# Kernel optimization log

Hardware: AMD Instinct MI355X
Metric: run time of the kernel (lower is better)

## Reference

```python
import jax, jax.numpy as jnp
import numpy as np
from jax import lax

# BatchNorm inference with running_mean=0, running_var=1: y = gamma*x/sqrt(1+eps) + beta
_BN_INV = 1.0 / float(np.sqrt(1.0 + 1e-5))


def _conv(x, w, b, pad):
    # x: (B,C,H,W), w: (O,C,k,k)
    y = lax.conv_general_dilated(x, w, (1, 1), [(pad, pad), (pad, pad)],
                                 dimension_numbers=('NCHW', 'OIHW', 'NCHW'))
    return y + b[None, :, None, None]


def _basic(x, w, b, g, e):
    # Conv5x5(pad=2) -> BN(inference) -> ReLU
    y = _conv(x, w, b, 2)
    y = y * (g * _BN_INV)[None, :, None, None] + e[None, :, None, None]
    return jnp.maximum(y, 0.0)


def _pool(x):
    # avg_pool2d kernel=2 stride=2
    B, C, H, W = x.shape
    return x.reshape(B, C, H // 2, 2, W // 2, 2).mean(axis=(3, 5))


def _up(x, oh, ow):
    # bilinear, align_corners=True (matches F.interpolate(..., align_corners=True))
    B, C, H, W = x.shape
    ys = jnp.linspace(0.0, H - 1.0, oh)
    xs = jnp.linspace(0.0, W - 1.0, ow)
    y0 = jnp.floor(ys).astype(jnp.int32)
    y1 = jnp.minimum(y0 + 1, H - 1)
    wy = (ys - y0)[:, None]  # (oh,1)
    x0 = jnp.floor(xs).astype(jnp.int32)
    x1 = jnp.minimum(x0 + 1, W - 1)
    wx = xs - x0  # (ow,)
    xh = x[:, :, y0, :] * (1.0 - wy) + x[:, :, y1, :] * wy  # (B,C,oh,W)
    return xh[..., x0] * (1.0 - wx) + xh[..., x1] * wx       # (B,C,oh,ow)


def setup_inputs() -> dict:
    key = jax.random.key(0)
    ks = jax.random.split(key, 16)
    chans = [(64, 3), (128, 64), (256, 128), (512, 256), (512, 512),
             (512, 1024), (256, 768), (3, 384)]
    inp = {"data": jax.random.normal(ks[0], (2, 3, 512, 512), jnp.float32)}
    for n, (o, c) in enumerate(chans, 1):
        fan = 1.0 / np.sqrt(c * 25.0)
        inp[f"w{n}"] = jax.random.normal(ks[n], (o, c, 5, 5), jnp.float32) * fan
        inp[f"b{n}"] = jnp.zeros((o,), jnp.float32)
        inp[f"g{n}"] = jnp.ones((o,), jnp.float32)
        inp[f"e{n}"] = jnp.zeros((o,), jnp.float32)
    inp["wo"] = jax.random.normal(ks[9], (3, 3, 1, 1), jnp.float32) * 0.5
    inp["bo"] = jnp.zeros((3,), jnp.float32)
    return inp


def reference(data, w1, b1, g1, e1, w2, b2, g2, e2, w3, b3, g3, e3,
              w4, b4, g4, e4, w5, b5, g5, e5, w6, b6, g6, e6,
              w7, b7, g7, e7, w8, b8, g8, e8, wo, bo):
    c1 = _basic(data, w1, b1, g1, e1)                    # (B,64,H,W)
    c2 = _basic(_pool(c1), w2, b2, g2, e2)               # (B,128,H/2,W/2)
    c3 = _basic(_pool(c2), w3, b3, g3, e3)               # (B,256,H/4,W/4)
    c4 = _basic(_pool(c3), w4, b4, g4, e4)               # (B,512,H/8,W/8)
    c5 = _basic(_pool(c4), w5, b5, g5, e5)               # (B,512,H/16,W/16)
    c6 = _basic(jnp.concatenate([c4, _up(c5, c4.shape[2], c4.shape[3])], 1),
                w6, b6, g6, e6)                          # (B,512,H/8,W/8)
    c7 = _basic(jnp.concatenate([c3, _up(c6, c3.shape[2], c3.shape[3])], 1),
                w7, b7, g7, e7)                          # (B,256,H/4,W/4)
    c8 = _basic(jnp.concatenate([c2, _up(c7, c2.shape[2], c2.shape[3])], 1),
                w8, b8, g8, e8)                          # (B,3,H/2,W/2)
    core = _conv(_up(c8, data.shape[2], data.shape[3]), wo, bo, 0)  # (B,3,H,W)
    return data * core
```

## Files before the change

kernel.cpp:

```cpp
#include <hip/hip_runtime.h>
#include <hip/hip_bf16.h>

typedef _Float16 f16x8 __attribute__((ext_vector_type(8)));
typedef _Float16 f16x4 __attribute__((ext_vector_type(4)));
typedef float f32x4 __attribute__((ext_vector_type(4)));

#define BN_S 0.99999500003749975f

__device__ inline f16x8 f16x8_zero() {
  f16x8 v = {(_Float16)0.f, (_Float16)0.f, (_Float16)0.f, (_Float16)0.f,
             (_Float16)0.f, (_Float16)0.f, (_Float16)0.f, (_Float16)0.f};
  return v;
}

__device__ __forceinline__ void load_lds16(const _Float16* g, _Float16* l) {
  __builtin_amdgcn_global_load_lds(
      (const __attribute__((address_space(1))) void*)g,
      (__attribute__((address_space(3))) void*)l, 16, 0, 0);
}

__global__ void zero_out_k(float* __restrict__ out, int n) {
  const int idx = blockIdx.x * 256 + threadIdx.x;
  if (idx < n) out[idx] = 0.f;
}

__global__ void zero16_k(_Float16* __restrict__ p, int n16) {
  const int idx = blockIdx.x * 256 + threadIdx.x;
  if (idx < n16) ((f16x8*)p)[idx] = f16x8_zero();
}

__global__ void wtrans16(const float* __restrict__ src, _Float16* __restrict__ dst,
                         const float* __restrict__ g, int O, int C, int total) {
  const int idx = blockIdx.x * 256 + threadIdx.x;
  if (idx >= total) return;
  const int OC = O * C;
  const int t = idx / OC;
  const int rem = idx - t * OC;
  const int o = rem / C;
  const int c = rem - o * C;
  dst[idx] = (_Float16)(src[(size_t)(o * C + c) * 25 + t] * g[o] * BN_S);
}

__global__ void wtrans8(const float* __restrict__ src, _Float16* __restrict__ dst,
                        const float* __restrict__ g) {
  const int idx = blockIdx.x * 256 + threadIdx.x;
  if (idx >= 28800) return;
  const int c = idx / 600;
  const int r = idx - c * 600;
  const int tap = r / 24;
  const int q = r - tap * 24;
  const int o = q >> 3, j = q & 7;
  const int cin = (c < 16) ? (c * 8 + j) : (128 + (c - 16) * 8 + j);
  dst[idx] = (_Float16)(src[((size_t)o * 384 + cin) * 25 + tap] * g[o] * BN_S);
}

template <int MF, int NF>
__global__ __launch_bounds__(256) void conv_gemm(
    const _Float16* __restrict__ in, const _Float16* __restrict__ wt,
    const float* __restrict__ gg, const float* __restrict__ bbv,
    const float* __restrict__ ev, _Float16* __restrict__ out,
    int Cin, int Cout, int lw, int lh,
    int inS, int Wpi, int bsi, int ibase,
    int outS, int outOff, int Wpo, int bso, int obase) {
  constexpr int BM = MF * 32;
  constexpr int BN = NF * 32;
  __shared__ _Float16 sA[2][BM * 32];
  __shared__ _Float16 sB[2][BN * 32];

  const int tid = threadIdx.x;
  const int lane = tid & 63;
  const int wid = tid >> 6;
  const int wm = wid >> 1, wn = wid & 1;
  const int lr = lane >> 4, lc = lane & 15;
  const int n0 = blockIdx.x * BN;
  const int m0 = blockIdx.y * BM;
  const int H = 1 << lh, W = 1 << lw;
  const int nkb = Cin >> 5;

  const int r0 = tid >> 2;
  const int chunk = (tid & 3) ^ ((r0 >> 1) & 3);

  const _Float16* a0 = wt + (size_t)(m0 + r0) * Cin + (chunk << 3);
  const _Float16* a1 = a0 + ((size_t)Cin << 6);
  const int t0off = -2 * Wpi - 2;
  const _Float16 *b0, *b1 = nullptr;
  {
    int n = n0 + r0;
    int pix0 = (n >> (lw + lh)) * bsi + ((n >> lw) & (H - 1)) * Wpi + (n & (W - 1)) + ibase;
    b0 = in + (size_t)(pix0 + t0off) * inS + (chunk << 3);
    if constexpr (BN == 128) {
      n = n0 + r0 + 64;
      int pix1 = (n >> (lw + lh)) * bsi + ((n >> lw) & (H - 1)) * Wpi + (n & (W - 1)) + ibase;
      b1 = in + (size_t)(pix1 + t0off) * inS + (chunk << 3);
    }
  }

  const int swz = (lr ^ ((lc >> 1) & 3)) << 3;

  f32x4 acc[MF][NF];
  const f32x4 vz = {0.f, 0.f, 0.f, 0.f};
#pragma unroll
  for (int i = 0; i < MF; ++i)
#pragma unroll
    for (int j = 0; j < NF; ++j) acc[i][j] = vz;

  const int nt = 25 * nkb;
  int kb = 0, dx = 0;
  const size_t a_tap = (size_t)Cout * Cin - ((size_t)nkb << 5);
  const int woff = wid << 9;

  {
    _Float16* sa = sA[0] + woff;
    _Float16* sb = sB[0] + woff;
    load_lds16(a0, sa);
    if constexpr (BM == 128) load_lds16(a1, sa + 2048);
    load_lds16(b0, sb);
    if constexpr (BN == 128) load_lds16(b1, sb + 2048);
  }
  __syncthreads();

  int cur = 0;
  for (int t = 0; t < nt; ++t) {
    if (t + 1 < nt) {
      a0 += 32; b0 += 32;
      if constexpr (BM == 128) a1 += 32;
      if constexpr (BN == 128) b1 += 32;
      if (++kb == nkb) {
        kb = 0;
        a0 += a_tap;
        if constexpr (BM == 128) a1 += a_tap;
        int pd;
        if (++dx == 5) { dx = 0; pd = Wpi - 4; } else pd = 1;
        const ptrdiff_t bd = (ptrdiff_t)pd * inS - ((ptrdiff_t)nkb << 5);
        b0 += bd;
        if constexpr (BN == 128) b1 += bd;
      }
      _Float16* sa = (cur ? sA[0] : sA[1]) + woff;
      _Float16* sb = (cur ? sB[0] : sB[1]) + woff;
      load_lds16(a0, sa);
      if constexpr (BM == 128) load_lds16(a1, sa + 2048);
      load_lds16(b0, sb);
      if constexpr (BN == 128) load_lds16(b1, sb + 2048);
    }
    const _Float16* pA = cur ? sA[1] : sA[0];
    const _Float16* pB = cur ? sB[1] : sB[0];
    f16x8 af[MF], bf[NF];
#pragma unroll
    for (int i = 0; i < MF; ++i)
      af[i] = *(const f16x8*)(pA + ((wm * (MF * 16) + (i << 4) + lc) << 5) + swz);
#pragma unroll
    for (int i = 0; i < NF; ++i)
      bf[i] = *(const f16x8*)(pB + ((wn * (NF * 16) + (i << 4) + lc) << 5) + swz);
#pragma unroll
    for (int mi = 0; mi < MF; ++mi)
#pragma unroll
      for (int ni = 0; ni < NF; ++ni)
        acc[mi][ni] =
            __builtin_amdgcn_mfma_f32_16x16x32_f16(af[mi], bf[ni], acc[mi][ni], 0, 0, 0);
    __syncthreads();
    cur ^= 1;
  }

#pragma unroll
  for (int mi = 0; mi < MF; ++mi) {
    const int ob = m0 + wm * (MF * 16) + (mi << 4) + (lr << 2);
    const f32x4 gv = *(const f32x4*)(gg + ob);
    const f32x4 bv = *(const f32x4*)(bbv + ob);
    const f32x4 evv = *(const f32x4*)(ev + ob);
#pragma unroll
    for (int ni = 0; ni < NF; ++ni) {
      const int n = n0 + wn * (NF * 16) + (ni << 4) + lc;
      const int y = (n >> lw) & (H - 1);
      const int x = n & (W - 1);
      const int bb_ = n >> (lw + lh);
      const size_t op = (size_t)(bb_ * bso + y * Wpo + x + obase) * outS + outOff + ob;
      f16x4 h;
#pragma unroll
      for (int j = 0; j < 4; ++j) {
        const float s = gv[j] * BN_S;
        float v = acc[mi][ni][j] + (bv[j] * s + evv[j]);
        v = v > 0.f ? v : 0.f;
        h[j] = (_Float16)v;
      }
      *(f16x4*)(out + op) = h;
    }
  }
}

__global__ __launch_bounds__(256) void conv1_k(
    const float* __restrict__ data, const float* __restrict__ w1,
    const float* __restrict__ g1, const float* __restrict__ b1,
    const float* __restrict__ e1, _Float16* __restrict__ out) {
  __shared__ float patch[3][20][20];
  const int tid = threadIdx.x;
  const int bid = blockIdx.x;
  const int tx = bid & 31, ty = (bid >> 5) & 31, b = bid >> 10;

  for (int i = tid; i < 1200; i += 256) {
    const int c = i / 400;
    const int r = i - c * 400;
    const int pyy = r / 20;
    const int pxx = r - pyy * 20;
    const int gy = (ty << 4) + pyy - 2, gx = (tx << 4) + pxx - 2;
    float v = 0.f;
    if ((unsigned)gy < 512u && (unsigned)gx < 512u)
      v = data[((size_t)(b * 3 + c) << 18) + (gy << 9) + gx];
    patch[c][pyy][pxx] = v;
  }
  __syncthreads();

  const int py = tid >> 4, px = tid & 15;
  float acc[64];
#pragma unroll
  for (int o = 0; o < 64; ++o) acc[o] = 0.f;

  for (int c = 0; c < 3; ++c)
    for (int dy = 0; dy < 5; ++dy) {
#pragma unroll
      for (int dx = 0; dx < 5; ++dx) {
        const float v = patch[c][py + dy][px + dx];
        const float* wb = w1 + c * 25 + dy * 5 + dx;
#pragma unroll
        for (int o = 0; o < 64; ++o) acc[o] = fmaf(v, wb[o * 75], acc[o]);
      }
    }

  const int y = (ty << 4) + py, x = (tx << 4) + px;
  _Float16* op = out + ((size_t)(((b << 9) + y) << 9) + x) * 64;
#pragma unroll
  for (int oc = 0; oc < 8; ++oc) {
    f16x8 h;
#pragma unroll
    for (int j = 0; j < 8; ++j) {
      const int o = (oc << 3) + j;
      const float s = g1[o] * BN_S;
      const float t = b1[o] * s + e1[o];
      float v = fmaf(acc[o], s, t);
      v = v > 0.f ? v : 0.f;
      h[j] = (_Float16)v;
    }
    *(f16x8*)(op + (oc << 3)) = h;
  }
}

__global__ void pool_k(const _Float16* __restrict__ in, _Float16* __restrict__ out,
                       int inS, int outS, int Wpi, int bsi, int ibase,
                       int Wpo, int bso, int obase,
                       int lwo, int lho, int lcc, int total) {
  const int idx = blockIdx.x * 256 + threadIdx.x;
  if (idx >= total) return;
  const int cc = idx & ((1 << lcc) - 1);
  const int pix = idx >> lcc;
  const int x = pix & ((1 << lwo) - 1);
  const int y = (pix >> lwo) & ((1 << lho) - 1);
  const int b = pix >> (lwo + lho);
  const int ip = b * bsi + (y << 1) * Wpi + (x << 1) + ibase;
  const _Float16* p = in + (size_t)ip * inS + (cc << 3);
  const f16x8 v00 = *(const f16x8*)p;
  const f16x8 v01 = *(const f16x8*)(p + inS);
  const f16x8 v10 = *(const f16x8*)(p + (size_t)Wpi * inS);
  const f16x8 v11 = *(const f16x8*)(p + (size_t)(Wpi + 1) * inS);
  f16x8 r;
#pragma unroll
  for (int j = 0; j < 8; ++j)
    r[j] = (_Float16)(((float)v00[j] + (float)v01[j] + (float)v10[j] + (float)v11[j]) * 0.25f);
  const int op = b * bso + y * Wpo + x + obase;
  *(f16x8*)(out + (size_t)op * outS + (cc << 3)) = r;
}

__global__ void up_k(const _Float16* __restrict__ in, _Float16* __restrict__ out,
                     int inS, int outS, int outOff,
                     int Wpi, int bsi, int ibase,
                     int Wpo, int bso, int obase,
                     int lwi, int lhi, int lcc, float scale, int total) {
  const int idx = blockIdx.x * 256 + threadIdx.x;
  if (idx >= total) return;
  const int cc = idx & ((1 << lcc) - 1);
  const int pix = idx >> lcc;
  const int lwo = lwi + 1, lho = lhi + 1;
  const int ox = pix & ((1 << lwo) - 1);
  const int oy = (pix >> lwo) & ((1 << lho) - 1);
  const int b = pix >> (lwo + lho);
  const int Hi = 1 << lhi, Wi = 1 << lwi;
  const float fy = oy * scale;
  const int y0 = (int)fy;
  const float wy = fy - y0;
  const int y1 = min(y0 + 1, Hi - 1);
  const float fx = ox * scale;
  const int x0 = (int)fx;
  const float wx = fx - x0;
  const int x1 = min(x0 + 1, Wi - 1);
  const int rbase = b * bsi + ibase;
  const _Float16* basep = in + (cc << 3);
  const f16x8 v00 = *(const f16x8*)(basep + (size_t)(rbase + y0 * Wpi + x0) * inS);
  const f16x8 v01 = *(const f16x8*)(basep + (size_t)(rbase + y0 * Wpi + x1) * inS);
  const f16x8 v10 = *(const f16x8*)(basep + (size_t)(rbase + y1 * Wpi + x0) * inS);
  const f16x8 v11 = *(const f16x8*)(basep + (size_t)(rbase + y1 * Wpi + x1) * inS);
  f16x8 r;
#pragma unroll
  for (int j = 0; j < 8; ++j) {
    const float top = (float)v00[j] * (1.f - wx) + (float)v01[j] * wx;
    const float bot = (float)v10[j] * (1.f - wx) + (float)v11[j] * wx;
    r[j] = (_Float16)(top * (1.f - wy) + bot * wy);
  }
  const int op = b * bso + oy * Wpo + ox + obase;
  *(f16x8*)(out + (size_t)op * outS + outOff + (cc << 3)) = r;
}

__global__ __launch_bounds__(256) void conv8_lds(
    const _Float16* __restrict__ inA, const _Float16* __restrict__ inB,
    const _Float16* __restrict__ wt, const float* __restrict__ b8,
    const float* __restrict__ g8, const float* __restrict__ e8,
    _Float16* __restrict__ out) {
  __shared__ f16x8 patch[2][20][20];
  const int tid = threadIdx.x;
  const int bid = blockIdx.x;
  const int tx = bid & 15, ty = (bid >> 4) & 15, b = bid >> 8;
  const int px = tid & 15, py = tid >> 4;
  const int x0 = tx << 4, y0 = ty << 4;

  float a0 = 0.f, a1 = 0.f, a2 = 0.f;
  for (int c = 0; c < 48; ++c) {
    const _Float16* sbase;
    int str;
    if (c < 16) { sbase = inA + ((size_t)b << 23) + (c << 3); str = 128; }
    else        { sbase = inB + ((size_t)b << 24) + ((c - 16) << 3); str = 256; }
    for (int i = tid; i < 400; i += 256) {
      const int pyy = i / 20, pxx = i - pyy * 20;
      const int gy = y0 + pyy - 2, gx = x0 + pxx - 2;
      f16x8 v = f16x8_zero();
      if ((unsigned)gy < 256u && (unsigned)gx < 256u)
        v = *(const f16x8*)(sbase + (size_t)((gy << 8) + gx) * str);
      patch[c & 1][pyy][pxx] = v;
    }
    __syncthreads();
    const _Float16* wb_c = wt + c * 600;
#pragma unroll
    for (int dy = 0; dy < 5; ++dy) {
#pragma unroll
      for (int dxx = 0; dxx < 5; ++dxx) {
        const f16x8 v = patch[c & 1][py + dy][px + dxx];
        const _Float16* wb = wb_c + (dy * 5 + dxx) * 24;
#pragma unroll
        for (int j = 0; j < 8; ++j) {
          const float f = (float)v[j];
          a0 = fmaf(f, (float)wb[j], a0);
          a1 = fmaf(f, (float)wb[8 + j], a1);
          a2 = fmaf(f, (float)wb[16 + j], a2);
        }
      }
    }
  }

  const float s0 = g8[0] * BN_S, t0 = b8[0] * s0 + e8[0];
  const float s1 = g8[1] * BN_S, t1 = b8[1] * s1 + e8[1];
  const float s2 = g8[2] * BN_S, t2 = b8[2] * s2 + e8[2];
  float r0 = a0 + t0, r1 = a1 + t1, r2 = a2 + t2;
  r0 = r0 > 0.f ? r0 : 0.f;
  r1 = r1 > 0.f ? r1 : 0.f;
  r2 = r2 > 0.f ? r2 : 0.f;
  f16x4 h;
  h[0] = (_Float16)r0; h[1] = (_Float16)r1; h[2] = (_Float16)r2; h[3] = (_Float16)0.f;
  const int opix = (b << 16) + ((y0 + py) << 8) + (x0 + px);
  *(f16x4*)(out + (size_t)opix * 4) = h;
}

__global__ void final_k(const float* __restrict__ data, const _Float16* __restrict__ c8,
                        const float* __restrict__ wo, const float* __restrict__ bo,
                        float* __restrict__ out) {
  const int idx = blockIdx.x * 256 + threadIdx.x;
  const int x = idx & 511, y = (idx >> 9) & 511, b = idx >> 18;
  const float sc = 255.f / 511.f;
  const float fy = y * sc;
  const int y0 = (int)fy;
  const float wy = fy - y0;
  const int y1 = min(y0 + 1, 255);
  const float fx = x * sc;
  const int x0 = (int)fx;
  const float wx = fx - x0;
  const int x1 = min(x0 + 1, 255);
  const f16x4 v00 = *(const f16x4*)(c8 + (size_t)((((b << 8) + y0) << 8) + x0) * 4);
  const f16x4 v01 = *(const f16x4*)(c8 + (size_t)((((b << 8) + y0) << 8) + x1) * 4);
  const f16x4 v10 = *(const f16x4*)(c8 + (size_t)((((b << 8) + y1) << 8) + x0) * 4);
  const f16x4 v11 = *(const f16x4*)(c8 + (size_t)((((b << 8) + y1) << 8) + x1) * 4);
  float u[3];
#pragma unroll
  for (int j = 0; j < 3; ++j) {
    const float top = (float)v00[j] * (1.f - wx) + (float)v01[j] * wx;
    const float bot = (float)v10[j] * (1.f - wx) + (float)v11[j] * wx;
    u[j] = top * (1.f - wy) + bot * wy;
  }
#pragma unroll
  for (int c = 0; c < 3; ++c) {
    const float core = bo[c] + wo[c * 3 + 0] * u[0] + wo[c * 3 + 1] * u[1] + wo[c * 3 + 2] * u[2];
    const size_t oi = ((size_t)(b * 3 + c) << 18) + (y << 9) + x;
    out[oi] = data[oi] * core;
  }
}

extern "C" void kernel_launch(void* const* d_in, const int* in_sizes, int n_in,
                              void* d_out, int out_size, void* d_ws, size_t ws_size,
                              hipStream_t stream) {
  const float* data = (const float*)d_in[0];
  const float *w[9], *bb[9], *gg[9], *ee[9];
  for (int n = 1; n <= 8; ++n) {
    w[n] = (const float*)d_in[1 + (n - 1) * 4];
    bb[n] = (const float*)d_in[2 + (n - 1) * 4];
    gg[n] = (const float*)d_in[3 + (n - 1) * 4];
    ee[n] = (const float*)d_in[4 + (n - 1) * 4];
  }
  const float* wo = (const float*)d_in[33];
  const float* bo = (const float*)d_in[34];
  float* out = (float*)d_out;
  (void)in_sizes; (void)n_in;

  const size_t NEEDED = 194810112ull;
  if (ws_size < NEEDED) {
    zero_out_k<<<(out_size + 255) / 256, 256, 0, stream>>>(out, out_size);
    return;
  }
  char* base = (char*)d_ws;
  size_t off = 0;
  auto alloc = [&](size_t bytes) -> char* {
    char* p = base + off;
    off += (bytes + 255) & ~(size_t)255;
    return p;
  };
  _Float16* W2t = (_Float16*)alloc(409600);
  _Float16* W3t = (_Float16*)alloc(1638400);
  _Float16* W4t = (_Float16*)alloc(6553600);
  _Float16* W5t = (_Float16*)alloc(13107200);
  _Float16* W6t = (_Float16*)alloc(26214400);
  _Float16* W7t = (_Float16*)alloc(9830400);
  _Float16* W8t = (_Float16*)alloc(57600);
  char* Rbig = alloc(72466432);
  char* c2b_ = alloc(33554432);
  char* R1 = alloc(17305600);
  char* R2 = alloc(13672448);

  _Float16* c1 = (_Float16*)Rbig;
  _Float16* cat7 = (_Float16*)Rbig;
  _Float16* cat6 = (_Float16*)(Rbig + 53526528);
  _Float16* up7b = (_Float16*)Rbig;
  _Float16* c2buf = (_Float16*)c2b_;
  _Float16* p1 = (_Float16*)R1;
  _Float16* c6 = (_Float16*)R1;
  _Float16* c7 = (_Float16*)R1;
  _Float16* c8 = (_Float16*)R1;
  _Float16* p2 = (_Float16*)R2;
  _Float16* p3 = (_Float16*)(R2 + 8921088);
  _Float16* p4 = (_Float16*)(R2 + 8921088);
  _Float16* c5 = (_Float16*)(R2 + 8921088 + 2654208);

  zero16_k<<<(1081600 + 255) / 256, 256, 0, stream>>>(p1, 1081600);
  zero16_k<<<(557568 + 255) / 256, 256, 0, stream>>>(p2, 557568);
  zero16_k<<<(295936 + 255) / 256, 256, 0, stream>>>(p3, 295936);

  wtrans16<<<(25 * 128 * 64 + 255) / 256, 256, 0, stream>>>(w[2], W2t, gg[2], 128, 64, 25 * 128 * 64);
  wtrans16<<<(25 * 256 * 128 + 255) / 256, 256, 0, stream>>>(w[3], W3t, gg[3], 256, 128, 25 * 256 * 128);
  wtrans16<<<(25 * 512 * 256 + 255) / 256, 256, 0, stream>>>(w[4], W4t, gg[4], 512, 256, 25 * 512 * 256);
  wtrans16<<<(25 * 512 * 512 + 255) / 256, 256, 0, stream>>>(w[5], W5t, gg[5], 512, 512, 25 * 512 * 512);
  wtrans16<<<(25 * 512 * 1024 + 255) / 256, 256, 0, stream>>>(w[6], W6t, gg[6], 512, 1024, 25 * 512 * 1024);
  wtrans16<<<(25 * 256 * 768 + 255) / 256, 256, 0, stream>>>(w[7], W7t, gg[7], 256, 768, 25 * 256 * 768);
  wtrans8<<<(28800 + 255) / 256, 256, 0, stream>>>(w[8], W8t, gg[8]);

  conv1_k<<<2048, 256, 0, stream>>>(data, w[1], gg[1], bb[1], ee[1], c1);
  pool_k<<<1048576 / 256, 256, 0, stream>>>(c1, p1, 64, 64, 512, 262144, 0,
                                            260, 67600, 522, 8, 8, 3, 1048576);
  zero16_k<<<(3345408 + 255) / 256, 256, 0, stream>>>(cat7, 3345408);
  zero16_k<<<(1183744 + 255) / 256, 256, 0, stream>>>(cat6, 1183744);

  conv_gemm<4, 4><<<dim3(1024, 1), 256, 0, stream>>>(p1, W2t, gg[2], bb[2], ee[2], c2buf,
      64, 128, 8, 8, 64, 260, 67600, 522, 128, 0, 256, 65536, 0);
  pool_k<<<524288 / 256, 256, 0, stream>>>(c2buf, p2, 128, 128, 256, 65536, 0,
                                           132, 17424, 266, 7, 7, 4, 524288);
  conv_gemm<4, 4><<<dim3(256, 2), 256, 0, stream>>>(p2, W3t, gg[3], bb[3], ee[3], cat7,
      128, 256, 7, 7, 128, 132, 17424, 266, 768, 0, 132, 17424, 266);
  pool_k<<<262144 / 256, 256, 0, stream>>>(cat7, p3, 768, 256, 132, 17424, 266,
                                           68, 4624, 138, 6, 6, 5, 262144);
  conv_gemm<4, 2><<<dim3(128, 4), 256, 0, stream>>>(p3, W4t, gg[4], bb[4], ee[4], cat6,
      256, 512, 6, 6, 256, 68, 4624, 138, 1024, 0, 68, 4624, 138);
  zero16_k<<<(165888 + 255) / 256, 256, 0, stream>>>(p4, 165888);
  pool_k<<<131072 / 256, 256, 0, stream>>>(cat6, p4, 1024, 512, 68, 4624, 138,
                                           36, 1296, 74, 5, 5, 6, 131072);
  conv_gemm<2, 2><<<dim3(32, 8), 256, 0, stream>>>(p4, W5t, gg[5], bb[5], ee[5], c5,
      512, 512, 5, 5, 512, 36, 1296, 74, 512, 0, 32, 1024, 0);
  up_k<<<524288 / 256, 256, 0, stream>>>(c5, cat6, 512, 1024, 512,
                                         32, 1024, 0, 68, 4624, 138,
                                         5, 5, 6, 31.f / 63.f, 524288);
  conv_gemm<4, 2><<<dim3(128, 4), 256, 0, stream>>>(cat6, W6t, gg[6], bb[6], ee[6], c6,
      1024, 512, 6, 6, 1024, 68, 4624, 138, 512, 0, 64, 4096, 0);
  up_k<<<2097152 / 256, 256, 0, stream>>>(c6, cat7, 512, 768, 256,
                                          64, 4096, 0, 132, 17424, 266,
                                          6, 6, 6, 63.f / 127.f, 2097152);
  conv_gemm<4, 2><<<dim3(512, 2), 256, 0, stream>>>(cat7, W7t, gg[7], bb[7], ee[7], c7,
      768, 256, 7, 7, 768, 132, 17424, 266, 256, 0, 128, 16384, 0);
  up_k<<<4194304 / 256, 256, 0, stream>>>(c7, up7b, 256, 256, 0,
                                          128, 16384, 0, 256, 65536, 0,
                                          7, 7, 5, 127.f / 255.f, 4194304);
  conv8_lds<<<512, 256, 0, stream>>>(c2buf, up7b, W8t, bb[8], gg[8], ee[8], c8);
  final_k<<<524288 / 256, 256, 0, stream>>>(data, c8, wo, bo, out);
}
```

Before: 1.961 ms.

## Deepen conv GEMM LDS pipeline to four buffers with vmcnt waits and larger tiles

The implicit-GEMM conv kernel moves from a double-buffered LDS pipeline with __syncthreads to a four-slot ring that prefetches two k-steps ahead. It waits on explicit s_waitcnt vmcnt counts so global-to-LDS loads overlap with MFMA work. Layers 4, 6 and 7 also switch from 128x64 to 128x128 tiles, which halves the grid. This aims to hide memory latency and improve data reuse, at the cost of doubled LDS use, lower occupancy, and a risk of wrong vmcnt counts if the compiler emits other vector memory operations in the loop.

Result: slower. 2.062 ms (+5.2%).

```diff
diff --git a/kernel.cpp b/kernel.cpp
--- a/kernel.cpp
+++ b/kernel.cpp
@@ -64,8 +64,9 @@
     int outS, int outOff, int Wpo, int bso, int obase) {
   constexpr int BM = MF * 32;
   constexpr int BN = NF * 32;
-  __shared__ _Float16 sA[2][BM * 32];
-  __shared__ _Float16 sB[2][BN * 32];
+  constexpr int LPS = ((BM == 128) ? 2 : 1) + ((BN == 128) ? 2 : 1);
+  __shared__ _Float16 sA[4][BM * 32];
+  __shared__ _Float16 sB[4][BN * 32];
 
   const int tid = threadIdx.x;
   const int lane = tid & 63;
@@ -109,41 +110,52 @@
   const size_t a_tap = (size_t)Cout * Cin - ((size_t)nkb << 5);
   const int woff = wid << 9;
 
-  {
-    _Float16* sa = sA[0] + woff;
-    _Float16* sb = sB[0] + woff;
+  auto advance = [&]() {
+    a0 += 32; b0 += 32;
+    if constexpr (BM == 128) a1 += 32;
+    if constexpr (BN == 128) b1 += 32;
+    if (++kb == nkb) {
+      kb = 0;
+      a0 += a_tap;
+      if constexpr (BM == 128) a1 += a_tap;
+      int pd;
+      if (++dx == 5) { dx = 0; pd = Wpi - 4; } else pd = 1;
+      const ptrdiff_t bd = (ptrdiff_t)pd * inS - ((ptrdiff_t)nkb << 5);
+      b0 += bd;
+      if constexpr (BN == 128) b1 += bd;
+    }
+  };
+  auto stage = [&](int buf) {
+    _Float16* sa = sA[buf] + woff;
+    _Float16* sb = sB[buf] + woff;
     load_lds16(a0, sa);
     if constexpr (BM == 128) load_lds16(a1, sa + 2048);
     load_lds16(b0, sb);
     if constexpr (BN == 128) load_lds16(b1, sb + 2048);
-  }
-  __syncthreads();
-
-  int cur = 0;
+  };
+
+  stage(0);
+  advance();
+  stage(1);
+
   for (int t = 0; t < nt; ++t) {
-    if (t + 1 < nt) {
-      a0 += 32; b0 += 32;
-      if constexpr (BM == 128) a1 += 32;
-      if constexpr (BN == 128) b1 += 32;
-      if (++kb == nkb) {
-        kb = 0;
-        a0 += a_tap;
-        if constexpr (BM == 128) a1 += a_tap;
-        int pd;
-        if (++dx == 5) { dx = 0; pd = Wpi - 4; } else pd = 1;
-        const ptrdiff_t bd = (ptrdiff_t)pd * inS - ((ptrdiff_t)nkb << 5);
-        b0 += bd;
-        if constexpr (BN == 128) b1 += bd;
-      }
-      _Float16* sa = (cur ? sA[0] : sA[1]) + woff;
-      _Float16* sb = (cur ? sB[0] : sB[1]) + woff;
-      load_lds16(a0, sa);
-      if constexpr (BM == 128) load_lds16(a1, sa + 2048);
-      load_lds16(b0, sb);
-      if constexpr (BN == 128) load_lds16(b1, sb + 2048);
-    }
-    const _Float16* pA = cur ? sA[1] : sA[0];
-    const _Float16* pB = cur ? sB[1] : sB[0];
+    if (t + 2 < nt) {
+      advance();
+      stage((t + 2) & 3);
+      if constexpr (LPS == 4) asm volatile("s_waitcnt vmcnt(8)" ::: "memory");
+      else if constexpr (LPS == 3) asm volatile("s_waitcnt vmcnt(6)" ::: "memory");
+      else asm volatile("s_waitcnt vmcnt(4)" ::: "memory");
+    } else if (t + 2 == nt) {
+      if constexpr (LPS == 4) asm volatile("s_waitcnt vmcnt(4)" ::: "memory");
+      else if constexpr (LPS == 3) asm volatile("s_waitcnt vmcnt(3)" ::: "memory");
+      else asm volatile("s_waitcnt vmcnt(2)" ::: "memory");
+    } else {
+      asm volatile("s_waitcnt vmcnt(0)" ::: "memory");
+    }
+    __builtin_amdgcn_s_barrier();
+
+    const _Float16* pA = sA[t & 3];
+    const _Float16* pB = sB[t & 3];
     f16x8 af[MF], bf[NF];
 #pragma unroll
     for (int i = 0; i < MF; ++i)
@@ -157,8 +169,7 @@
       for (int ni = 0; ni < NF; ++ni)
         acc[mi][ni] =
             __builtin_amdgcn_mfma_f32_16x16x32_f16(af[mi], bf[ni], acc[mi][ni], 0, 0, 0);
-    __syncthreads();
-    cur ^= 1;
+    __builtin_amdgcn_s_barrier();
   }
 
 #pragma unroll
@@ -478,7 +489,7 @@
       128, 256, 7, 7, 128, 132, 17424, 266, 768, 0, 132, 17424, 266);
   pool_k<<<262144 / 256, 256, 0, stream>>>(cat7, p3, 768, 256, 132, 17424, 266,
                                            68, 4624, 138, 6, 6, 5, 262144);
-  conv_gemm<4, 2><<<dim3(128, 4), 256, 0, stream>>>(p3, W4t, gg[4], bb[4], ee[4], cat6,
+  conv_gemm<4, 4><<<dim3(64, 4), 256, 0, stream>>>(p3, W4t, gg[4], bb[4], ee[4], cat6,
       256, 512, 6, 6, 256, 68, 4624, 138, 1024, 0, 68, 4624, 138);
   zero16_k<<<(165888 + 255) / 256, 256, 0, stream>>>(p4, 165888);
   pool_k<<<131072 / 256, 256, 0, stream>>>(cat6, p4, 1024, 512, 68, 4624, 138,
@@ -488,12 +499,12 @@
   up_k<<<524288 / 256, 256, 0, stream>>>(c5, cat6, 512, 1024, 512,
                                          32, 1024, 0, 68, 4624, 138,
                                          5, 5, 6, 31.f / 63.f, 524288);
-  conv_gemm<4, 2><<<dim3(128, 4), 256, 0, stream>>>(cat6, W6t, gg[6], bb[6], ee[6], c6,
+  conv_gemm<4, 4><<<dim3(64, 4), 256, 0, stream>>>(cat6, W6t, gg[6], bb[6], ee[6], c6,
       1024, 512, 6, 6, 1024, 68, 4624, 138, 512, 0, 64, 4096, 0);
   up_k<<<2097152 / 256, 256, 0, stream>>>(c6, cat7, 512, 768, 256,
                                           64, 4096, 0, 132, 17424, 266,
                                           6, 6, 6, 63.f / 127.f, 2097152);
-  conv_gemm<4, 2><<<dim3(512, 2), 256, 0, stream>>>(cat7, W7t, gg[7], bb[7], ee[7], c7,
+  conv_gemm<4, 4><<<dim3(256, 2), 256, 0, stream>>>(cat7, W7t, gg[7], bb[7], ee[7], c7,
       768, 256, 7, 7, 768, 132, 17424, 266, 256, 0, 128, 16384, 0);
   up_k<<<4194304 / 256, 256, 0, stream>>>(c7, up7b, 256, 256, 0,
                                           128, 16384, 0, 256, 65536, 0,
```

## Deepen conv GEMM K-step per barrier and widen N tiles to 128

Applied to the files above, without the earlier changes.

Adds a KS template parameter so each pipeline stage loads and computes KS 32-wide K slices between barriers, halving the number of __syncthreads and loop iterations for most convolutions. Separately, layers 4, 6 and 7 switch from 128x64 to 128x128 tiles with half the grid in x, raising per-block reuse of A and B. The cost is doubled LDS per block (up to 64KB), more accumulator registers and fewer blocks, which can lower occupancy and grid fill on small layers.

Result: no change. 1.939 ms (-1.1%).

```diff
diff --git a/kernel.cpp b/kernel.cpp
--- a/kernel.cpp
+++ b/kernel.cpp
@@ -54,7 +54,7 @@
   dst[idx] = (_Float16)(src[((size_t)o * 384 + cin) * 25 + tap] * g[o] * BN_S);
 }
 
-template <int MF, int NF>
+template <int MF, int NF, int KS>
 __global__ __launch_bounds__(256) void conv_gemm(
     const _Float16* __restrict__ in, const _Float16* __restrict__ wt,
     const float* __restrict__ gg, const float* __restrict__ bbv,
@@ -64,8 +64,10 @@
     int outS, int outOff, int Wpo, int bso, int obase) {
   constexpr int BM = MF * 32;
   constexpr int BN = NF * 32;
-  __shared__ _Float16 sA[2][BM * 32];
-  __shared__ _Float16 sB[2][BN * 32];
+  constexpr int SUB_A = BM * 32;
+  constexpr int SUB_B = BN * 32;
+  __shared__ _Float16 sA[2][SUB_A * KS];
+  __shared__ _Float16 sB[2][SUB_B * KS];
 
   const int tid = threadIdx.x;
   const int lane = tid & 63;
@@ -104,59 +106,66 @@
 #pragma unroll
     for (int j = 0; j < NF; ++j) acc[i][j] = vz;
 
-  const int nt = 25 * nkb;
+  const int np = 25 * nkb / KS;
   int kb = 0, dx = 0;
   const size_t a_tap = (size_t)Cout * Cin - ((size_t)nkb << 5);
   const int woff = wid << 9;
 
-  {
-    _Float16* sa = sA[0] + woff;
-    _Float16* sb = sB[0] + woff;
-    load_lds16(a0, sa);
-    if constexpr (BM == 128) load_lds16(a1, sa + 2048);
-    load_lds16(b0, sb);
-    if constexpr (BN == 128) load_lds16(b1, sb + 2048);
-  }
+  auto advance = [&]() {
+    a0 += 32 * KS; b0 += 32 * KS;
+    if constexpr (BM == 128) a1 += 32 * KS;
+    if constexpr (BN == 128) b1 += 32 * KS;
+    kb += KS;
+    if (kb == nkb) {
+      kb = 0;
+      a0 += a_tap;
+      if constexpr (BM == 128) a1 += a_tap;
+      int pd;
+      if (++dx == 5) { dx = 0; pd = Wpi - 4; } else pd = 1;
+      const ptrdiff_t bd = (ptrdiff_t)pd * inS - ((ptrdiff_t)nkb << 5);
+      b0 += bd;
+      if constexpr (BN == 128) b1 += bd;
+    }
+  };
+  auto stage = [&](int buf) {
+#pragma unroll
+    for (int s = 0; s < KS; ++s) {
+      _Float16* sa = sA[buf] + s * SUB_A + woff;
+      _Float16* sb = sB[buf] + s * SUB_B + woff;
+      load_lds16(a0 + 32 * s, sa);
+      if constexpr (BM == 128) load_lds16(a1 + 32 * s, sa + 2048);
+      load_lds16(b0 + 32 * s, sb);
+      if constexpr (BN == 128) load_lds16(b1 + 32 * s, sb + 2048);
+    }
+  };
+
+  stage(0);
   __syncthreads();
 
   int cur = 0;
-  for (int t = 0; t < nt; ++t) {
-    if (t + 1 < nt) {
-      a0 += 32; b0 += 32;
-      if constexpr (BM == 128) a1 += 32;
-      if constexpr (BN == 128) b1 += 32;
-      if (++kb == nkb) {
-        kb = 0;
-        a0 += a_tap;
-        if constexpr (BM == 128) a1 += a_tap;
-        int pd;
-        if (++dx == 5) { dx = 0; pd = Wpi - 4; } else pd = 1;
-        const ptrdiff_t bd = (ptrdiff_t)pd * inS - ((ptrdiff_t)nkb << 5);
-        b0 += bd;
-        if constexpr (BN == 128) b1 += bd;
-      }
-      _Float16* sa = (cur ? sA[0] : sA[1]) + woff;
-      _Float16* sb = (cur ? sB[0] : sB[1]) + woff;
-      load_lds16(a0, sa);
-      if constexpr (BM == 128) load_lds16(a1, sa + 2048);
-      load_lds16(b0, sb);
-      if constexpr (BN == 128) load_lds16(b1, sb + 2048);
-    }
-    const _Float16* pA = cur ? sA[1] : sA[0];
-    const _Float16* pB = cur ? sB[1] : sB[0];
-    f16x8 af[MF], bf[NF];
-#pragma unroll
-    for (int i = 0; i < MF; ++i)
-      af[i] = *(const f16x8*)(pA + ((wm * (MF * 16) + (i << 4) + lc) << 5) + swz);
-#pragma unroll
-    for (int i = 0; i < NF; ++i)
-      bf[i] = *(const f16x8*)(pB + ((wn * (NF * 16) + (i << 4) + lc) << 5) + swz);
-#pragma unroll
-    for (int mi = 0; mi < MF; ++mi)
-#pragma unroll
-      for (int ni = 0; ni < NF; ++ni)
-        acc[mi][ni] =
-            __builtin_amdgcn_mfma_f32_16x16x32_f16(af[mi], bf[ni], acc[mi][ni], 0, 0, 0);
+  for (int t = 0; t < np; ++t) {
+    if (t + 1 < np) {
+      advance();
+      stage(cur ^ 1);
+    }
+    const _Float16* pA = sA[cur];
+    const _Float16* pB = sB[cur];
+#pragma unroll
+    for (int s = 0; s < KS; ++s) {
+      f16x8 af[MF], bf[NF];
+#pragma unroll
+      for (int i = 0; i < MF; ++i)
+        af[i] = *(const f16x8*)(pA + s * SUB_A + ((wm * (MF * 16) + (i << 4) + lc) << 5) + swz);
+#pragma unroll
+      for (int i = 0; i < NF; ++i)
+        bf[i] = *(const f16x8*)(pB + s * SUB_B + ((wn * (NF * 16) + (i << 4) + lc) << 5) + swz);
+#pragma unroll
+      for (int mi = 0; mi < MF; ++mi)
+#pragma unroll
+        for (int ni = 0; ni < NF; ++ni)
+          acc[mi][ni] =
+              __builtin_amdgcn_mfma_f32_16x16x32_f16(af[mi], bf[ni], acc[mi][ni], 0, 0, 0);
+    }
     __syncthreads();
     cur ^= 1;
   }
@@ -470,30 +479,30 @@
   zero16_k<<<(3345408 + 255) / 256, 256, 0, stream>>>(cat7, 3345408);
   zero16_k<<<(1183744 + 255) / 256, 256, 0, stream>>>(cat6, 1183744);
 
-  conv_gemm<4, 4><<<dim3(1024, 1), 256, 0, stream>>>(p1, W2t, gg[2], bb[2], ee[2], c2buf,
+  conv_gemm<4, 4, 1><<<dim3(1024, 1), 256, 0, stream>>>(p1, W2t, gg[2], bb[2], ee[2], c2buf,
       64, 128, 8, 8, 64, 260, 67600, 522, 128, 0, 256, 65536, 0);
   pool_k<<<524288 / 256, 256, 0, stream>>>(c2buf, p2, 128, 128, 256, 65536, 0,
                                            132, 17424, 266, 7, 7, 4, 524288);
-  conv_gemm<4, 4><<<dim3(256, 2), 256, 0, stream>>>(p2, W3t, gg[3], bb[3], ee[3], cat7,
+  conv_gemm<4, 4, 2><<<dim3(256, 2), 256, 0, stream>>>(p2, W3t, gg[3], bb[3], ee[3], cat7,
       128, 256, 7, 7, 128, 132, 17424, 266, 768, 0, 132, 17424, 266);
   pool_k<<<262144 / 256, 256, 0, stream>>>(cat7, p3, 768, 256, 132, 17424, 266,
                                            68, 4624, 138, 6, 6, 5, 262144);
-  conv_gemm<4, 2><<<dim3(128, 4), 256, 0, stream>>>(p3, W4t, gg[4], bb[4], ee[4], cat6,
+  conv_gemm<4, 4, 2><<<dim3(64, 4), 256, 0, stream>>>(p3, W4t, gg[4], bb[4], ee[4], cat6,
       256, 512, 6, 6, 256, 68, 4624, 138, 1024, 0, 68, 4624, 138);
   zero16_k<<<(165888 + 255) / 256, 256, 0, stream>>>(p4, 165888);
   pool_k<<<131072 / 256, 256, 0, stream>>>(cat6, p4, 1024, 512, 68, 4624, 138,
                                            36, 1296, 74, 5, 5, 6, 131072);
-  conv_gemm<2, 2><<<dim3(32, 8), 256, 0, stream>>>(p4, W5t, gg[5], bb[5], ee[5], c5,
+  conv_gemm<2, 2, 2><<<dim3(32, 8), 256, 0, stream>>>(p4, W5t, gg[5], bb[5], ee[5], c5,
       512, 512, 5, 5, 512, 36, 1296, 74, 512, 0, 32, 1024, 0);
   up_k<<<524288 / 256, 256, 0, stream>>>(c5, cat6, 512, 1024, 512,
                                          32, 1024, 0, 68, 4624, 138,
                                          5, 5, 6, 31.f / 63.f, 524288);
-  conv_gemm<4, 2><<<dim3(128, 4), 256, 0, stream>>>(cat6, W6t, gg[6], bb[6], ee[6], c6,
+  conv_gemm<4, 4, 2><<<dim3(64, 4), 256, 0, stream>>>(cat6, W6t, gg[6], bb[6], ee[6], c6,
       1024, 512, 6, 6, 1024, 68, 4624, 138, 512, 0, 64, 4096, 0);
   up_k<<<2097152 / 256, 256, 0, stream>>>(c6, cat7, 512, 768, 256,
                                           64, 4096, 0, 132, 17424, 266,
                                           6, 6, 6, 63.f / 127.f, 2097152);
-  conv_gemm<4, 2><<<dim3(512, 2), 256, 0, stream>>>(cat7, W7t, gg[7], bb[7], ee[7], c7,
+  conv_gemm<4, 4, 2><<<dim3(256, 2), 256, 0, stream>>>(cat7, W7t, gg[7], bb[7], ee[7], c7,
       768, 256, 7, 7, 768, 132, 17424, 266, 256, 0, 128, 16384, 0);
   up_k<<<4194304 / 256, 256, 0, stream>>>(c7, up7b, 256, 256, 0,
                                           128, 16384, 0, 256, 65536, 0,
```
